# Kernel optimization log

Hardware: AMD Instinct MI355X
Metric: run time of the kernel (lower is better)

The kernel has to match this reference:

```python
import jax, jax.numpy as jnp
import numpy as np


def pixel_unshuffle(x, r):
    # torch.nn.PixelUnshuffle: 'b c (h r1) (w r2) -> b (c r1 r2) h w'
    b, c, h, w = x.shape
    x = x.reshape(b, c, h // r, r, w // r, r)
    x = x.transpose(0, 1, 3, 5, 2, 4)
    return x.reshape(b, c * r * r, h // r, w // r)


def conv2d_same(x, w, groups=1):
    # 3x3, stride 1, padding 1, no bias
    return jax.lax.conv_general_dilated(
        x, w, window_strides=(1, 1), padding=[(1, 1), (1, 1)],
        dimension_numbers=('NCHW', 'OIHW', 'NCHW'),
        feature_group_count=groups)


def setup_inputs() -> dict:
    key = jax.random.key(0)
    k1, k2, k3, k4 = jax.random.split(key, 4)
    n_feat = 96
    B, H, W = 8, 256, 256
    x = jax.random.normal(k1, (B, n_feat, H, W), dtype=jnp.float32)
    mask = jax.random.normal(k2, (B, 1, H, W), dtype=jnp.float32)
    # body conv: Conv2d(n_feat, n_feat//2, 3, padding=1, bias=False)
    w_body = jax.random.normal(k3, (n_feat // 2, n_feat, 3, 3), dtype=jnp.float32) * 0.02
    # proj conv: Conv2d(4*n_feat, 2*n_feat, 3, groups=2*n_feat, bias=False) -> per-group in=2, out=1
    w_proj = jax.random.normal(k4, (n_feat * 2, 2, 3, 3), dtype=jnp.float32) * 0.02
    return {'x': x, 'mask': mask, 'w_body': w_body, 'w_proj': w_proj}


def reference(x, mask, w_body, w_proj):
    # body: conv -> pixel_unshuffle(2): [B, 2*n_feat, H/2, W/2]
    out = pixel_unshuffle(conv2d_same(x, w_body), 2)
    # body2: pixel_unshuffle(2) on 1-channel mask: [B, 4, H/2, W/2]
    out_mask = pixel_unshuffle(mask, 2)
    b, n, h, w = out.shape
    # interleave: even channels = out[i], odd channels = out_mask[i % 4]
    om = out_mask[:, jnp.arange(n) % 4]            # [B, n, h, w]
    t = jnp.stack([out, om], axis=2).reshape(b, 2 * n, h, w)
    groups = w_proj.shape[0]                        # = 2*n_feat
    return conv2d_same(t, w_proj, groups=groups)
```

## Files before the change

kernel.cpp:

```cpp
#include <hip/hip_runtime.h>
#include <hip/hip_bf16.h>
#include <cstddef>
#include <cstdint>

#define B_   8
#define CIN  96
#define H_   256
#define W_   256
#define CO1  48
#define NCH  192
#define HO   128
#define WO   128

#define IMG   50176
#define IMGV  (IMG / 16)
#define LDS1  (3 * IMG)

typedef short  v8s __attribute__((ext_vector_type(8)));
typedef float  v4f __attribute__((ext_vector_type(4)));

static __device__ __forceinline__ unsigned short f2bf(float f) {
    __hip_bfloat16 h = __float2bfloat16(f);
    return *(unsigned short*)&h;
}
static __device__ __forceinline__ float bf2f(unsigned short u) {
    return __uint_as_float(((unsigned int)u) << 16);
}

__global__ void prep_weights(const float* __restrict__ wb, unsigned short* __restrict__ wbf2) {
    int o = blockIdx.x * blockDim.x + threadIdx.x;
    if (o >= 81 * 512) return;
    int f = o >> 9, r = o & 511;
    int lane = r >> 3, e = r & 7;
    int l4 = lane >> 4, l15 = lane & 15;
    int mf = f % 3, ks = (f / 3) % 3, tap = f / 9;
    int co = mf * 16 + l15;
    int ci = ks * 32 + l4 * 8 + e;
    wbf2[o] = f2bf(wb[(co * CIN + ci) * 9 + tap]);
}

__global__ __launch_bounds__(256) void transpose_x(const float* __restrict__ x,
                                                   char* __restrict__ xt) {
    extern __shared__ char lds[];
    const int ri = blockIdx.x;
    const int b  = blockIdx.y;
    const int t  = threadIdx.x;

#pragma unroll
    for (int k = 0; k < 13; ++k) {
        int s = t + 256 * k;
        if (s < IMGV) ((uint4*)lds)[s] = make_uint4(0u, 0u, 0u, 0u);
    }
    __syncthreads();

    const int h = ri - 1;
    if (0 <= h && h < 256) {
        const float* xp = x + (((size_t)b * CIN) << 16) + (h << 8) + t;
        const int px = t + 1;
        char* cbase = lds + px * 192;
        const int s = px & 3;
#pragma unroll
        for (int c = 0; c < 12; ++c) {
            float f[8];
#pragma unroll
            for (int j = 0; j < 8; ++j)
                f[j] = xp[((size_t)(8 * c + j)) << 16];
            uint4 d;
            d.x = f2bf(f[0]) | ((unsigned)f2bf(f[1]) << 16);
            d.y = f2bf(f[2]) | ((unsigned)f2bf(f[3]) << 16);
            d.z = f2bf(f[4]) | ((unsigned)f2bf(f[5]) << 16);
            d.w = f2bf(f[6]) | ((unsigned)f2bf(f[7]) << 16);
            *(uint4*)(cbase + ((c ^ s) << 4)) = d;
        }
    }
    __syncthreads();

    const uint4* sp = (const uint4*)lds;
    uint4* dp = (uint4*)(xt + ((size_t)b * 258 + ri) * IMG);
#pragma unroll
    for (int k = 0; k < 13; ++k) {
        int s = t + 256 * k;
        if (s < IMGV) dp[s] = sp[s];
    }
}

static __device__ __forceinline__ void dma_row(char* lds_base, const char* gsrc,
                                               int wv, int lane) {
    const int k0 = wv * 13;
    const int k1 = (k0 + 13 < 49) ? (k0 + 13) : 49;
    for (int k = k0; k < k1; ++k) {
        __builtin_amdgcn_global_load_lds(
            (const __attribute__((address_space(1))) unsigned int*)(gsrc + k * 1024 + lane * 16),
            (__attribute__((address_space(3))) unsigned int*)(lds_base + k * 1024),
            16, 0, 0);
    }
}

static __device__ __forceinline__ void kh_block(const char* bb0, const char* apl,
                                                int kh, const unsigned* U, v4f* acc) {
#pragma unroll
    for (int kw = 0; kw < 3; ++kw) {
        const char* bb = bb0 + U[kw];
#pragma unroll
        for (int ks = 0; ks < 3; ++ks) {
            const int f0 = ((kh * 3 + kw) * 3 + ks) * 3;
            v8s a0 = *(const v8s*)(apl + (f0 + 0) * 1024);
            v8s a1 = *(const v8s*)(apl + (f0 + 1) * 1024);
            v8s a2 = *(const v8s*)(apl + (f0 + 2) * 1024);
            v8s b0 = *(const v8s*)(bb + ks * 64 + 0 * 3072);
            v8s b1 = *(const v8s*)(bb + ks * 64 + 1 * 3072);
            v8s b2 = *(const v8s*)(bb + ks * 64 + 2 * 3072);
            v8s b3 = *(const v8s*)(bb + ks * 64 + 3 * 3072);
            acc[0]  = __builtin_amdgcn_mfma_f32_16x16x32_bf16(a0, b0, acc[0],  0, 0, 0);
            acc[1]  = __builtin_amdgcn_mfma_f32_16x16x32_bf16(a0, b1, acc[1],  0, 0, 0);
            acc[2]  = __builtin_amdgcn_mfma_f32_16x16x32_bf16(a0, b2, acc[2],  0, 0, 0);
            acc[3]  = __builtin_amdgcn_mfma_f32_16x16x32_bf16(a0, b3, acc[3],  0, 0, 0);
            acc[4]  = __builtin_amdgcn_mfma_f32_16x16x32_bf16(a1, b0, acc[4],  0, 0, 0);
            acc[5]  = __builtin_amdgcn_mfma_f32_16x16x32_bf16(a1, b1, acc[5],  0, 0, 0);
            acc[6]  = __builtin_amdgcn_mfma_f32_16x16x32_bf16(a1, b2, acc[6],  0, 0, 0);
            acc[7]  = __builtin_amdgcn_mfma_f32_16x16x32_bf16(a1, b3, acc[7],  0, 0, 0);
            acc[8]  = __builtin_amdgcn_mfma_f32_16x16x32_bf16(a2, b0, acc[8],  0, 0, 0);
            acc[9]  = __builtin_amdgcn_mfma_f32_16x16x32_bf16(a2, b1, acc[9],  0, 0, 0);
            acc[10] = __builtin_amdgcn_mfma_f32_16x16x32_bf16(a2, b2, acc[10], 0, 0, 0);
            acc[11] = __builtin_amdgcn_mfma_f32_16x16x32_bf16(a2, b3, acc[11], 0, 0, 0);
        }
    }
}

__global__ __launch_bounds__(256) void conv1_dma(const char* __restrict__ xt,
                                                 const unsigned short* __restrict__ wbf2,
                                                 unsigned short* __restrict__ y_us) {
    extern __shared__ char lds[];
    const int band = blockIdx.x;
    const int b    = blockIdx.y;
    const int h0   = band * 8;
    const int tid  = threadIdx.x;
    const int lane = tid & 63;
    const int wv   = tid >> 6;
    const int l15  = lane & 15;
    const int l4   = lane >> 4;
    const int w0   = wv * 64;

    const char* apl    = (const char*)wbf2 + lane * 16;
    const char* xrows  = xt + (size_t)b * 258 * IMG;

    unsigned U[3];
#pragma unroll
    for (int kw = 0; kw < 3; ++kw) {
        int p = w0 + l15 + kw;
        U[kw] = (unsigned)(p * 192 + ((l4 ^ (p & 3)) << 4));
    }

    char* s0 = lds;
    char* s1 = lds + IMG;
    char* s2 = lds + 2 * IMG;

    dma_row(s0, xrows + (size_t)(h0)     * IMG, wv, lane);
    dma_row(s1, xrows + (size_t)(h0 + 1) * IMG, wv, lane);
    asm volatile("s_waitcnt vmcnt(0)" ::: "memory");
    __builtin_amdgcn_s_barrier();
    dma_row(s2, xrows + (size_t)(h0 + 2) * IMG, wv, lane);

#pragma unroll 1
    for (int i = 0; i < 8; ++i) {
        const int h = h0 + i;
        v4f acc[12];
#pragma unroll
        for (int k = 0; k < 12; ++k) acc[k] = (v4f){0.f, 0.f, 0.f, 0.f};

        kh_block(s0, apl, 0, U, acc);
        kh_block(s1, apl, 1, U, acc);

        asm volatile("s_waitcnt vmcnt(0)" ::: "memory");
        __builtin_amdgcn_s_barrier();
        __builtin_amdgcn_sched_barrier(0);

        if (i < 7)
            dma_row(s0, xrows + (size_t)(h + 3) * IMG, wv, lane);

        kh_block(s2, apl, 2, U, acc);

        const int dy = h & 1, hp1 = h >> 1;
#pragma unroll
        for (int mf = 0; mf < 3; ++mf) {
#pragma unroll
            for (int nf = 0; nf < 4; ++nf) {
                const int Wp = w0 + nf * 16 + l15;
                const int dx = Wp & 1, wq = Wp >> 1;
#pragma unroll
                for (int r = 0; r < 4; ++r) {
                    const int co = mf * 16 + l4 * 4 + r;
                    const int n  = co * 4 + dy * 2 + dx;
                    y_us[(((size_t)b * NCH + n) << 14) + (hp1 << 7) + wq] =
                        f2bf(acc[mf * 4 + nf][r]);
                }
            }
        }

        char* tmp = s0; s0 = s1; s1 = s2; s2 = tmp;
    }
}

#define T2H 16
__global__ __launch_bounds__(256) void conv2_kernel(
    const unsigned short* __restrict__ y_us, const float* __restrict__ mask,
    const float* __restrict__ wproj, float* __restrict__ out)
{
    __shared__ unsigned short yt[(T2H + 2) * 132];
    __shared__ float          mt[(T2H + 2) * 132];

    const int tid  = threadIdx.x;
    const int bid  = blockIdx.x;
    const int band = bid & 7;
    const int bn   = bid >> 3;
    const int b    = bn / NCH;
    const int n    = bn - b * NCH;
    const int h0   = band * T2H;
    const int q    = n & 3, dy = q >> 1, dx = q & 1;

    const unsigned short* yc = y_us + ((size_t)bn << 14);
    const float*          mk = mask + ((size_t)b << 16);

#pragma unroll
    for (int k = 0; k < 10; ++k) {
        int idx = tid + 256 * k;
        if (idx < (T2H + 2) * 132) {
            int ly = idx / 132;
            int lx = idx - ly * 132;
            int gy = h0 - 1 + ly, gx = lx - 1;
            bool ok = ((unsigned)gy < (unsigned)HO) && ((unsigned)gx < (unsigned)WO)
                      && (lx < 130);
            yt[idx] = ok ? yc[(gy << 7) + gx] : (unsigned short)0;
            mt[idx] = ok ? mk[((2 * gy + dy) << 8) + (2 * gx + dx)] : 0.f;
        }
    }
    __syncthreads();

    const float* wp = wproj + n * 18;
    float wy[9], wm[9];
#pragma unroll
    for (int j = 0; j < 9; ++j) { wy[j] = wp[j]; wm[j] = wp[9 + j]; }

    const int tx = tid & 127;
    const int tz = tid >> 7;
    const int rbase = tz * 8;

    float y0[3], y1[3], m0[3], m1[3];
#pragma unroll
    for (int kw = 0; kw < 3; ++kw) {
        y0[kw] = bf2f(yt[(rbase + 0) * 132 + tx + kw]);
        m0[kw] = mt[(rbase + 0) * 132 + tx + kw];
        y1[kw] = bf2f(yt[(rbase + 1) * 132 + tx + kw]);
        m1[kw] = mt[(rbase + 1) * 132 + tx + kw];
    }

#pragma unroll
    for (int i = 0; i < 8; ++i) {
        float y2[3], m2[3];
#pragma unroll
        for (int kw = 0; kw < 3; ++kw) {
            y2[kw] = bf2f(yt[(rbase + i + 2) * 132 + tx + kw]);
            m2[kw] = mt[(rbase + i + 2) * 132 + tx + kw];
        }
        float acc = 0.f;
#pragma unroll
        for (int kw = 0; kw < 3; ++kw) {
            acc = fmaf(wy[0 * 3 + kw], y0[kw], acc);
            acc = fmaf(wm[0 * 3 + kw], m0[kw], acc);
        }
#pragma unroll
        for (int kw = 0; kw < 3; ++kw) {
            acc = fmaf(wy[1 * 3 + kw], y1[kw], acc);
            acc = fmaf(wm[1 * 3 + kw], m1[kw], acc);
        }
#pragma unroll
        for (int kw = 0; kw < 3; ++kw) {
            acc = fmaf(wy[2 * 3 + kw], y2[kw], acc);
            acc = fmaf(wm[2 * 3 + kw], m2[kw], acc);
        }
        const int oy = h0 + rbase + i;
        out[((size_t)bn << 14) + (oy << 7) + tx] = acc;
#pragma unroll
        for (int kw = 0; kw < 3; ++kw) {
            y0[kw] = y1[kw]; y1[kw] = y2[kw];
            m0[kw] = m1[kw]; m1[kw] = m2[kw];
        }
    }
}

extern "C" void kernel_launch(void* const* d_in, const int* in_sizes, int n_in,
                              void* d_out, int out_size, void* d_ws, size_t ws_size,
                              hipStream_t stream) {
    const float* x      = (const float*)d_in[0];
    const float* mask   = (const float*)d_in[1];
    const float* w_body = (const float*)d_in[2];
    const float* w_proj = (const float*)d_in[3];
    float* out = (float*)d_out;

    char* p = (char*)d_ws;
    unsigned short* wbf2 = (unsigned short*)p;   p += (81 * 512 * 2 + 255) & ~255ull;
    char*           xt   = p;                    p += ((size_t)B_ * 258 * IMG + 255) & ~255ull;
    unsigned short* y_us = (unsigned short*)p;

    (void)hipFuncSetAttribute(reinterpret_cast<const void*>(conv1_dma),
                              hipFuncAttributeMaxDynamicSharedMemorySize, LDS1);

    {   int nel = 81 * 512;
        prep_weights<<<(nel + 255) / 256, 256, 0, stream>>>(w_body, wbf2); }
    {   dim3 grid(258, B_);
        transpose_x<<<grid, 256, IMG, stream>>>(x, xt); }
    {   dim3 grid(32, B_);
        conv1_dma<<<grid, 256, LDS1, stream>>>(xt, wbf2, y_us); }
    {   conv2_kernel<<<B_ * NCH * (HO / T2H), 256, 0, stream>>>(y_us, mask, w_proj, out); }
}
```

Before: 429.8 us.

## Fuse input transpose into conv1 and share mask tiles across channels in conv2

Removes the separate transpose_x pass and its bf16 intermediate buffer. conv1 now reads fp32 x directly, converts it to bf16 into a swizzled LDS ring, and prefetches the next row into registers while the MFMAs run. The block grows to 512 threads with half the N-tile per wave. conv2 now handles four channels that share the same mask phase per block, so each mask tile is loaded once and reused four times. In exchange, the strided fp32 global loads sit inside conv1, and two barriers per row are added.

```diff
diff --git a/kernel.cpp b/kernel.cpp
--- a/kernel.cpp
+++ b/kernel.cpp
@@ -12,9 +12,8 @@
 #define HO   128
 #define WO   128
 
-#define IMG   50176
-#define IMGV  (IMG / 16)
-#define LDS1  (3 * IMG)
+#define SLOT  49536
+#define LDS1  (3 * SLOT)
 
 typedef short  v8s __attribute__((ext_vector_type(8)));
 typedef float  v4f __attribute__((ext_vector_type(4)));
@@ -39,65 +38,35 @@
     wbf2[o] = f2bf(wb[(co * CIN + ci) * 9 + tap]);
 }
 
-__global__ __launch_bounds__(256) void transpose_x(const float* __restrict__ x,
-                                                   char* __restrict__ xt) {
-    extern __shared__ char lds[];
-    const int ri = blockIdx.x;
-    const int b  = blockIdx.y;
-    const int t  = threadIdx.x;
-
-#pragma unroll
-    for (int k = 0; k < 13; ++k) {
-        int s = t + 256 * k;
-        if (s < IMGV) ((uint4*)lds)[s] = make_uint4(0u, 0u, 0u, 0u);
-    }
-    __syncthreads();
-
-    const int h = ri - 1;
-    if (0 <= h && h < 256) {
-        const float* xp = x + (((size_t)b * CIN) << 16) + (h << 8) + t;
-        const int px = t + 1;
-        char* cbase = lds + px * 192;
-        const int s = px & 3;
-#pragma unroll
-        for (int c = 0; c < 12; ++c) {
-            float f[8];
-#pragma unroll
-            for (int j = 0; j < 8; ++j)
-                f[j] = xp[((size_t)(8 * c + j)) << 16];
-            uint4 d;
-            d.x = f2bf(f[0]) | ((unsigned)f2bf(f[1]) << 16);
-            d.y = f2bf(f[2]) | ((unsigned)f2bf(f[3]) << 16);
-            d.z = f2bf(f[4]) | ((unsigned)f2bf(f[5]) << 16);
-            d.w = f2bf(f[6]) | ((unsigned)f2bf(f[7]) << 16);
-            *(uint4*)(cbase + ((c ^ s) << 4)) = d;
-        }
-    }
-    __syncthreads();
-
-    const uint4* sp = (const uint4*)lds;
-    uint4* dp = (uint4*)(xt + ((size_t)b * 258 + ri) * IMG);
-#pragma unroll
-    for (int k = 0; k < 13; ++k) {
-        int s = t + 256 * k;
-        if (s < IMGV) dp[s] = sp[s];
-    }
-}
-
-static __device__ __forceinline__ void dma_row(char* lds_base, const char* gsrc,
-                                               int wv, int lane) {
-    const int k0 = wv * 13;
-    const int k1 = (k0 + 13 < 49) ? (k0 + 13) : 49;
-    for (int k = k0; k < k1; ++k) {
-        __builtin_amdgcn_global_load_lds(
-            (const __attribute__((address_space(1))) unsigned int*)(gsrc + k * 1024 + lane * 16),
-            (__attribute__((address_space(3))) unsigned int*)(lds_base + k * 1024),
-            16, 0, 0);
-    }
-}
-
-static __device__ __forceinline__ void kh_block(const char* bb0, const char* apl,
-                                                int kh, const unsigned* U, v4f* acc) {
+static __device__ __forceinline__ void stage_load(const float* __restrict__ xb, int r,
+                                                  int c, int q, float4* f) {
+    const bool rok = ((unsigned)r < 256u);
+    const float* g = xb + (((size_t)(c << 3)) << 16) + (r << 8) + (q << 2);
+#pragma unroll
+    for (int e = 0; e < 8; ++e)
+        f[e] = rok ? *(const float4*)(g + (((size_t)e) << 16))
+                   : make_float4(0.f, 0.f, 0.f, 0.f);
+}
+
+static __device__ __forceinline__ void stage_write(char* __restrict__ slot,
+                                                   int c, int q, const float4* f) {
+    const float* fp = (const float*)f;
+#pragma unroll
+    for (int k = 0; k < 4; ++k) {
+        const int px = 4 * q + 1 + k;
+        const unsigned ad = (unsigned)(px * 192 + ((c ^ ((1 + k) & 3)) << 4));
+        uint4 d;
+        d.x = f2bf(fp[0 * 4 + k]) | ((unsigned)f2bf(fp[1 * 4 + k]) << 16);
+        d.y = f2bf(fp[2 * 4 + k]) | ((unsigned)f2bf(fp[3 * 4 + k]) << 16);
+        d.z = f2bf(fp[4 * 4 + k]) | ((unsigned)f2bf(fp[5 * 4 + k]) << 16);
+        d.w = f2bf(fp[6 * 4 + k]) | ((unsigned)f2bf(fp[7 * 4 + k]) << 16);
+        *(uint4*)(slot + ad) = d;
+    }
+}
+
+static __device__ __forceinline__ void kh_block2(const char* __restrict__ bb0,
+                                                 const char* __restrict__ apl,
+                                                 int kh, const unsigned* U, v4f* acc) {
 #pragma unroll
     for (int kw = 0; kw < 3; ++kw) {
         const char* bb = bb0 + U[kw];
@@ -107,84 +76,96 @@
             v8s a0 = *(const v8s*)(apl + (f0 + 0) * 1024);
             v8s a1 = *(const v8s*)(apl + (f0 + 1) * 1024);
             v8s a2 = *(const v8s*)(apl + (f0 + 2) * 1024);
-            v8s b0 = *(const v8s*)(bb + ks * 64 + 0 * 3072);
-            v8s b1 = *(const v8s*)(bb + ks * 64 + 1 * 3072);
-            v8s b2 = *(const v8s*)(bb + ks * 64 + 2 * 3072);
-            v8s b3 = *(const v8s*)(bb + ks * 64 + 3 * 3072);
-            acc[0]  = __builtin_amdgcn_mfma_f32_16x16x32_bf16(a0, b0, acc[0],  0, 0, 0);
-            acc[1]  = __builtin_amdgcn_mfma_f32_16x16x32_bf16(a0, b1, acc[1],  0, 0, 0);
-            acc[2]  = __builtin_amdgcn_mfma_f32_16x16x32_bf16(a0, b2, acc[2],  0, 0, 0);
-            acc[3]  = __builtin_amdgcn_mfma_f32_16x16x32_bf16(a0, b3, acc[3],  0, 0, 0);
-            acc[4]  = __builtin_amdgcn_mfma_f32_16x16x32_bf16(a1, b0, acc[4],  0, 0, 0);
-            acc[5]  = __builtin_amdgcn_mfma_f32_16x16x32_bf16(a1, b1, acc[5],  0, 0, 0);
-            acc[6]  = __builtin_amdgcn_mfma_f32_16x16x32_bf16(a1, b2, acc[6],  0, 0, 0);
-            acc[7]  = __builtin_amdgcn_mfma_f32_16x16x32_bf16(a1, b3, acc[7],  0, 0, 0);
-            acc[8]  = __builtin_amdgcn_mfma_f32_16x16x32_bf16(a2, b0, acc[8],  0, 0, 0);
-            acc[9]  = __builtin_amdgcn_mfma_f32_16x16x32_bf16(a2, b1, acc[9],  0, 0, 0);
-            acc[10] = __builtin_amdgcn_mfma_f32_16x16x32_bf16(a2, b2, acc[10], 0, 0, 0);
-            acc[11] = __builtin_amdgcn_mfma_f32_16x16x32_bf16(a2, b3, acc[11], 0, 0, 0);
-        }
-    }
-}
-
-__global__ __launch_bounds__(256) void conv1_dma(const char* __restrict__ xt,
-                                                 const unsigned short* __restrict__ wbf2,
-                                                 unsigned short* __restrict__ y_us) {
+            v8s b0 = *(const v8s*)(bb + ks * 64);
+            v8s b1 = *(const v8s*)(bb + ks * 64 + 3072);
+            acc[0] = __builtin_amdgcn_mfma_f32_16x16x32_bf16(a0, b0, acc[0], 0, 0, 0);
+            acc[1] = __builtin_amdgcn_mfma_f32_16x16x32_bf16(a0, b1, acc[1], 0, 0, 0);
+            acc[2] = __builtin_amdgcn_mfma_f32_16x16x32_bf16(a1, b0, acc[2], 0, 0, 0);
+            acc[3] = __builtin_amdgcn_mfma_f32_16x16x32_bf16(a1, b1, acc[3], 0, 0, 0);
+            acc[4] = __builtin_amdgcn_mfma_f32_16x16x32_bf16(a2, b0, acc[4], 0, 0, 0);
+            acc[5] = __builtin_amdgcn_mfma_f32_16x16x32_bf16(a2, b1, acc[5], 0, 0, 0);
+        }
+    }
+}
+
+__global__ __launch_bounds__(512) void conv1_direct(const float* __restrict__ x,
+                                                    const unsigned short* __restrict__ wbf2,
+                                                    unsigned short* __restrict__ y_us) {
     extern __shared__ char lds[];
     const int band = blockIdx.x;
     const int b    = blockIdx.y;
     const int h0   = band * 8;
     const int tid  = threadIdx.x;
     const int lane = tid & 63;
-    const int wv   = tid >> 6;
     const int l15  = lane & 15;
     const int l4   = lane >> 4;
-    const int w0   = wv * 64;
-
-    const char* apl    = (const char*)wbf2 + lane * 16;
-    const char* xrows  = xt + (size_t)b * 258 * IMG;
+    const int w0   = (tid >> 6) * 32;
+
+    const char*  apl = (const char*)wbf2 + lane * 16;
+    const float* xb  = x + (((size_t)b * CIN) << 16);
+
+    const int c1 = tid >> 6, q1 = lane;
+    const bool two = (tid < 256);
+    const int c2 = 8 + (tid >> 6);
 
     unsigned U[3];
 #pragma unroll
     for (int kw = 0; kw < 3; ++kw) {
-        int p = w0 + l15 + kw;
+        const int p = w0 + l15 + kw;
         U[kw] = (unsigned)(p * 192 + ((l4 ^ (p & 3)) << 4));
     }
 
     char* s0 = lds;
-    char* s1 = lds + IMG;
-    char* s2 = lds + 2 * IMG;
-
-    dma_row(s0, xrows + (size_t)(h0)     * IMG, wv, lane);
-    dma_row(s1, xrows + (size_t)(h0 + 1) * IMG, wv, lane);
-    asm volatile("s_waitcnt vmcnt(0)" ::: "memory");
-    __builtin_amdgcn_s_barrier();
-    dma_row(s2, xrows + (size_t)(h0 + 2) * IMG, wv, lane);
-
+    char* s1 = lds + SLOT;
+    char* s2 = lds + 2 * SLOT;
+
+    if (tid < 72) {
+        int s = tid / 24, rem = tid % 24;
+        int c = rem % 12, px = (rem / 12) * 257;
+        *(uint4*)(lds + s * SLOT + px * 192 + ((c ^ (px & 3)) << 4)) =
+            make_uint4(0u, 0u, 0u, 0u);
+    }
+
+    {
+        float4 f[8];
+#pragma unroll
+        for (int pr = 0; pr < 3; ++pr) {
+            const int r = h0 - 1 + pr;
+            char* slot = lds + pr * SLOT;
+            stage_load(xb, r, c1, q1, f);
+            stage_write(slot, c1, q1, f);
+            if (two) {
+                stage_load(xb, r, c2, q1, f);
+                stage_write(slot, c2, q1, f);
+            }
+        }
+    }
+    __syncthreads();
+
+    float4 stA[8], stB[8];
 #pragma unroll 1
     for (int i = 0; i < 8; ++i) {
         const int h = h0 + i;
-        v4f acc[12];
-#pragma unroll
-        for (int k = 0; k < 12; ++k) acc[k] = (v4f){0.f, 0.f, 0.f, 0.f};
-
-        kh_block(s0, apl, 0, U, acc);
-        kh_block(s1, apl, 1, U, acc);
-
-        asm volatile("s_waitcnt vmcnt(0)" ::: "memory");
-        __builtin_amdgcn_s_barrier();
-        __builtin_amdgcn_sched_barrier(0);
-
-        if (i < 7)
-            dma_row(s0, xrows + (size_t)(h + 3) * IMG, wv, lane);
-
-        kh_block(s2, apl, 2, U, acc);
+        const bool do_stage = (i < 7);
+
+        if (do_stage) {
+            stage_load(xb, h + 2, c1, q1, stA);
+            if (two) stage_load(xb, h + 2, c2, q1, stB);
+        }
+
+        v4f acc[6];
+#pragma unroll
+        for (int k = 0; k < 6; ++k) acc[k] = (v4f){0.f, 0.f, 0.f, 0.f};
+
+        kh_block2(s0, apl, 0, U, acc);
+        kh_block2(s1, apl, 1, U, acc);
+        kh_block2(s2, apl, 2, U, acc);
 
         const int dy = h & 1, hp1 = h >> 1;
 #pragma unroll
         for (int mf = 0; mf < 3; ++mf) {
 #pragma unroll
-            for (int nf = 0; nf < 4; ++nf) {
+            for (int nf = 0; nf < 2; ++nf) {
                 const int Wp = w0 + nf * 16 + l15;
                 const int dx = Wp & 1, wq = Wp >> 1;
 #pragma unroll
@@ -192,98 +173,132 @@
                     const int co = mf * 16 + l4 * 4 + r;
                     const int n  = co * 4 + dy * 2 + dx;
                     y_us[(((size_t)b * NCH + n) << 14) + (hp1 << 7) + wq] =
-                        f2bf(acc[mf * 4 + nf][r]);
+                        f2bf(acc[mf * 2 + nf][r]);
                 }
             }
         }
 
+        __syncthreads();
+        if (do_stage) {
+            stage_write(s0, c1, q1, stA);
+            if (two) stage_write(s0, c2, q1, stB);
+        }
+        __syncthreads();
         char* tmp = s0; s0 = s1; s1 = s2; s2 = tmp;
     }
 }
 
 #define T2H 16
-__global__ __launch_bounds__(256) void conv2_kernel(
+__global__ __launch_bounds__(256) void conv2_v2(
     const unsigned short* __restrict__ y_us, const float* __restrict__ mask,
     const float* __restrict__ wproj, float* __restrict__ out)
 {
-    __shared__ unsigned short yt[(T2H + 2) * 132];
     __shared__ float          mt[(T2H + 2) * 132];
+    __shared__ unsigned short yt[4][(T2H + 2) * 132];
 
     const int tid  = threadIdx.x;
     const int bid  = blockIdx.x;
     const int band = bid & 7;
-    const int bn   = bid >> 3;
-    const int b    = bn / NCH;
-    const int n    = bn - b * NCH;
+    const int t1   = bid >> 3;
+    const int g    = t1 % 12;
+    const int t2   = t1 / 12;
+    const int q    = t2 & 3;
+    const int b    = t2 >> 2;
     const int h0   = band * T2H;
-    const int q    = n & 3, dy = q >> 1, dx = q & 1;
-
-    const unsigned short* yc = y_us + ((size_t)bn << 14);
-    const float*          mk = mask + ((size_t)b << 16);
-
-#pragma unroll
-    for (int k = 0; k < 10; ++k) {
-        int idx = tid + 256 * k;
-        if (idx < (T2H + 2) * 132) {
-            int ly = idx / 132;
-            int lx = idx - ly * 132;
-            int gy = h0 - 1 + ly, gx = lx - 1;
-            bool ok = ((unsigned)gy < (unsigned)HO) && ((unsigned)gx < (unsigned)WO)
-                      && (lx < 130);
-            yt[idx] = ok ? yc[(gy << 7) + gx] : (unsigned short)0;
-            mt[idx] = ok ? mk[((2 * gy + dy) << 8) + (2 * gx + dx)] : 0.f;
+    const int dy   = q >> 1, dx = q & 1;
+
+    const int tx = tid & 127;
+    const int ty = tid >> 7;
+
+    const float* mk = mask + ((size_t)b << 16);
+    for (int ly = ty; ly < T2H + 2; ly += 2) {
+        const int gy = h0 - 1 + ly;
+        const bool rok = ((unsigned)gy < (unsigned)HO);
+        {
+            const int lx = tx, gx = lx - 1;
+            const bool ok = rok && ((unsigned)gx < (unsigned)WO);
+            mt[ly * 132 + lx] = ok ? mk[((2 * gy + dy) << 8) + (2 * gx + dx)] : 0.f;
+        }
+        if (tx < 2) {
+            const int lx = 128 + tx, gx = lx - 1;
+            const bool ok = rok && ((unsigned)gx < (unsigned)WO);
+            mt[ly * 132 + lx] = ok ? mk[((2 * gy + dy) << 8) + (2 * gx + dx)] : 0.f;
+        }
+    }
+
+#pragma unroll
+    for (int p = 0; p < 4; ++p) {
+        const int n = 16 * g + 4 * p + q;
+        const unsigned short* yc = y_us + ((size_t)(b * NCH + n) << 14);
+        for (int ly = ty; ly < T2H + 2; ly += 2) {
+            const int gy = h0 - 1 + ly;
+            const bool rok = ((unsigned)gy < (unsigned)HO);
+            {
+                const int lx = tx, gx = lx - 1;
+                const bool ok = rok && ((unsigned)gx < (unsigned)WO);
+                yt[p][ly * 132 + lx] = ok ? yc[(gy << 7) + gx] : (unsigned short)0;
+            }
+            if (tx < 2) {
+                const int lx = 128 + tx, gx = lx - 1;
+                const bool ok = rok && ((unsigned)gx < (unsigned)WO);
+                yt[p][ly * 132 + lx] = ok ? yc[(gy << 7) + gx] : (unsigned short)0;
+            }
         }
     }
     __syncthreads();
 
-    const float* wp = wproj + n * 18;
-    float wy[9], wm[9];
-#pragma unroll
-    for (int j = 0; j < 9; ++j) { wy[j] = wp[j]; wm[j] = wp[9 + j]; }
-
-    const int tx = tid & 127;
-    const int tz = tid >> 7;
-    const int rbase = tz * 8;
-
-    float y0[3], y1[3], m0[3], m1[3];
-#pragma unroll
-    for (int kw = 0; kw < 3; ++kw) {
-        y0[kw] = bf2f(yt[(rbase + 0) * 132 + tx + kw]);
-        m0[kw] = mt[(rbase + 0) * 132 + tx + kw];
-        y1[kw] = bf2f(yt[(rbase + 1) * 132 + tx + kw]);
-        m1[kw] = mt[(rbase + 1) * 132 + tx + kw];
-    }
-
-#pragma unroll
-    for (int i = 0; i < 8; ++i) {
-        float y2[3], m2[3];
+    const int rbase = ty * 8;
+
+#pragma unroll
+    for (int p = 0; p < 4; ++p) {
+        const int n = 16 * g + 4 * p + q;
+        const float* wp = wproj + n * 18;
+        float wy[9], wm[9];
+#pragma unroll
+        for (int j = 0; j < 9; ++j) { wy[j] = wp[j]; wm[j] = wp[9 + j]; }
+
+        const unsigned short* ytp = yt[p];
+
+        float y0[3], y1[3], m0[3], m1[3];
 #pragma unroll
         for (int kw = 0; kw < 3; ++kw) {
-            y2[kw] = bf2f(yt[(rbase + i + 2) * 132 + tx + kw]);
-            m2[kw] = mt[(rbase + i + 2) * 132 + tx + kw];
-        }
-        float acc = 0.f;
-#pragma unroll
-        for (int kw = 0; kw < 3; ++kw) {
-            acc = fmaf(wy[0 * 3 + kw], y0[kw], acc);
-            acc = fmaf(wm[0 * 3 + kw], m0[kw], acc);
-        }
-#pragma unroll
-        for (int kw = 0; kw < 3; ++kw) {
-            acc = fmaf(wy[1 * 3 + kw], y1[kw], acc);
-            acc = fmaf(wm[1 * 3 + kw], m1[kw], acc);
-        }
-#pragma unroll
-        for (int kw = 0; kw < 3; ++kw) {
-            acc = fmaf(wy[2 * 3 + kw], y2[kw], acc);
-            acc = fmaf(wm[2 * 3 + kw], m2[kw], acc);
-        }
-        const int oy = h0 + rbase + i;
-        out[((size_t)bn << 14) + (oy << 7) + tx] = acc;
-#pragma unroll
-        for (int kw = 0; kw < 3; ++kw) {
-            y0[kw] = y1[kw]; y1[kw] = y2[kw];
-            m0[kw] = m1[kw]; m1[kw] = m2[kw];
+            y0[kw] = bf2f(ytp[(rbase + 0) * 132 + tx + kw]);
+            m0[kw] = mt[(rbase + 0) * 132 + tx + kw];
+            y1[kw] = bf2f(ytp[(rbase + 1) * 132 + tx + kw]);
+            m1[kw] = mt[(rbase + 1) * 132 + tx + kw];
+        }
+
+#pragma unroll
+        for (int i = 0; i < 8; ++i) {
+            float y2[3], m2[3];
+#pragma unroll
+            for (int kw = 0; kw < 3; ++kw) {
+                y2[kw] = bf2f(ytp[(rbase + i + 2) * 132 + tx + kw]);
+                m2[kw] = mt[(rbase + i + 2) * 132 + tx + kw];
+            }
+            float acc = 0.f;
+#pragma unroll
+            for (int kw = 0; kw < 3; ++kw) {
+                acc = fmaf(wy[0 * 3 + kw], y0[kw], acc);
+                acc = fmaf(wm[0 * 3 + kw], m0[kw], acc);
+            }
+#pragma unroll
+            for (int kw = 0; kw < 3; ++kw) {
+                acc = fmaf(wy[1 * 3 + kw], y1[kw], acc);
+                acc = fmaf(wm[1 * 3 + kw], m1[kw], acc);
+            }
+#pragma unroll
+            for (int kw = 0; kw < 3; ++kw) {
+                acc = fmaf(wy[2 * 3 + kw], y2[kw], acc);
+                acc = fmaf(wm[2 * 3 + kw], m2[kw], acc);
+            }
+            const int oy = h0 + rbase + i;
+            out[((size_t)(b * NCH + n) << 14) + (oy << 7) + tx] = acc;
+#pragma unroll
+            for (int kw = 0; kw < 3; ++kw) {
+                y0[kw] = y1[kw]; y1[kw] = y2[kw];
+                m0[kw] = m1[kw]; m1[kw] = m2[kw];
+            }
         }
     }
 }
@@ -299,17 +314,14 @@
 
     char* p = (char*)d_ws;
     unsigned short* wbf2 = (unsigned short*)p;   p += (81 * 512 * 2 + 255) & ~255ull;
-    char*           xt   = p;                    p += ((size_t)B_ * 258 * IMG + 255) & ~255ull;
     unsigned short* y_us = (unsigned short*)p;
 
-    (void)hipFuncSetAttribute(reinterpret_cast<const void*>(conv1_dma),
+    (void)hipFuncSetAttribute(reinterpret_cast<const void*>(conv1_direct),
                               hipFuncAttributeMaxDynamicSharedMemorySize, LDS1);
 
     {   int nel = 81 * 512;
         prep_weights<<<(nel + 255) / 256, 256, 0, stream>>>(w_body, wbf2); }
-    {   dim3 grid(258, B_);
-        transpose_x<<<grid, 256, IMG, stream>>>(x, xt); }
     {   dim3 grid(32, B_);
-        conv1_dma<<<grid, 256, LDS1, stream>>>(xt, wbf2, y_us); }
-    {   conv2_kernel<<<B_ * NCH * (HO / T2H), 256, 0, stream>>>(y_us, mask, w_proj, out); }
-}
+        conv1_direct<<<grid, 512, LDS1, stream>>>(x, wbf2, y_us); }
+    {   conv2_v2<<<B_ * 4 * 12 * (HO / T2H), 256, 0, stream>>>(y_us, mask, w_proj, out); }
+}
```

Result: slower. 564.8 us (+31.4%).
